# Kernel tuning notes

Hardware: AMD Instinct MI355X
Metric: run time of the kernel (lower is better)

## Reference

```python
import jax, jax.numpy as jnp
import numpy as np

H = 16            # num_heads
WIN = 512         # window_size
G = 64            # num_global_tokens
MAXPOS = 8192


def setup_inputs() -> dict:
    key = jax.random.key(0)
    ks = jax.random.split(key, 9)
    B, S, D = 4, 4096, 1024
    s = 1.0 / np.sqrt(D)
    return {
        "x": jax.random.normal(ks[0], (B, S, D), jnp.float32),
        "pos_emb": jax.random.normal(ks[1], (MAXPOS, D), jnp.float32) * 0.02,
        "global_memory": jax.random.normal(ks[2], (1, G, D), jnp.float32),
        "conv_w": jax.random.normal(ks[3], (D, D, 4), jnp.float32) * s,   # (out_ch, in_ch, k)
        "conv_b": jax.random.normal(ks[4], (D,), jnp.float32) * 0.01,
        "gate_w": jax.random.normal(ks[5], (2 * D, D), jnp.float32) * s,  # (in, out)
        "gate_b": jnp.zeros((D,), jnp.float32),
        "out_w": jax.random.normal(ks[6], (D, D), jnp.float32) * s,
        "out_b": jnp.zeros((D,), jnp.float32),
    }


def reference(x, pos_emb, global_memory, conv_w, conv_b, gate_w, gate_b, out_w, out_b):
    B, S, D = x.shape
    hd = D // H
    scale = 1.0 / np.sqrt(hd)

    # positional encoding (seq <= max_position)
    x = x + pos_emb[:S][None]

    # ---- sliding window attention (non-overlapping windows, q=k=v=x) ----
    pad = (-S) % WIN
    xp = jnp.pad(x, ((0, 0), (0, pad), (0, 0))) if pad else x
    nW = xp.shape[1] // WIN
    w = xp.reshape(B, nW, WIN, H, hd)                                  # [B,nW,W,H,hd]
    attn = jnp.einsum('bnqhd,bnkhd->bnhqk', w, w) * scale
    attn = jax.nn.softmax(attn, axis=-1)
    local = jnp.einsum('bnhqk,bnkhd->bnqhd', attn, w)
    local = local.reshape(B, nW * WIN, D)[:, :S]                       # [B,S,D]

    # ---- compressed global attention ----
    comp = jax.lax.conv_general_dilated(
        x.transpose(0, 2, 1), conv_w, window_strides=(4,), padding='VALID',
        dimension_numbers=('NCH', 'OIH', 'NCH')) + conv_b[None, :, None]
    comp = comp.transpose(0, 2, 1)[:, :G]                              # [B,G,D]
    gt = jnp.concatenate([comp, jnp.broadcast_to(global_memory, (B, G, D))], axis=1)
    gt = gt.reshape(B, 2 * G, H, hd)                                   # [B,2G,H,hd]
    xm = x.reshape(B, S, H, hd)
    ga = jax.nn.softmax(jnp.einsum('bshd,bghd->bhsg', xm, gt) * scale, axis=-1)
    glob = jnp.einsum('bhsg,bghd->bshd', ga, gt).reshape(B, S, D)      # [B,S,D]

    # ---- gated mix + output projection (dropout disabled / eval) ----
    mix = jax.nn.sigmoid(jnp.concatenate([local, glob], axis=-1) @ gate_w + gate_b)
    out = mix * local + (1.0 - mix) * glob
    return out @ out_w + out_b
```

## Files before the change

### kernel.cpp

```cpp
#include <hip/hip_runtime.h>
#include <math.h>

#define B 4
#define S 4096
#define D 1024
#define H 16
#define HD 64
#define WIN 512
#define NW 8
#define G 64
#define G2 128
#define SCALE 0.125f

typedef __attribute__((ext_vector_type(8))) short bf16x8;
typedef __attribute__((ext_vector_type(4))) float f32x4;

__device__ inline unsigned short f2bf(float f) {
    unsigned u = __builtin_bit_cast(unsigned, f);
    return (unsigned short)((u + 0x7FFFu + ((u >> 16) & 1u)) >> 16);
}

__device__ inline float bf2f(unsigned short u) {
    return __builtin_bit_cast(float, (unsigned)u << 16);
}

__device__ inline unsigned long long pack4bf(float a, float b, float c, float d) {
    return (unsigned long long)f2bf(a) | ((unsigned long long)f2bf(b) << 16) |
           ((unsigned long long)f2bf(c) << 32) | ((unsigned long long)f2bf(d) << 48);
}

__device__ inline void gload16(const void* g, void* l) {
    __builtin_amdgcn_global_load_lds(
        (const __attribute__((address_space(1))) unsigned*)g,
        (__attribute__((address_space(3))) unsigned*)l, 16, 0, 0);
}

#define LDS_FENCE() asm volatile("" ::: "memory")

__global__ void k_posadd(const float* __restrict__ x, const float* __restrict__ pos,
                         float* __restrict__ xe) {
    int i = blockIdx.x * blockDim.x + threadIdx.x;
    float4 xv = ((const float4*)x)[i];
    int e = i & (S * D / 4 - 1);
    float4 pv = ((const float4*)pos)[e];
    xv.x += pv.x; xv.y += pv.y; xv.z += pv.z; xv.w += pv.w;
    ((float4*)xe)[i] = xv;
}

template <int KD>
__global__ void k_wtrans(const float* __restrict__ w, unsigned short* __restrict__ wT) {
    __shared__ float tile[32][33];
    int k0 = blockIdx.x * 32, n0 = blockIdx.y * 32;
    int tx = threadIdx.x & 31, ty = threadIdx.x >> 5;
#pragma unroll
    for (int i = 0; i < 4; ++i)
        tile[ty + 8 * i][tx] = w[(size_t)(k0 + ty + 8 * i) * 1024 + n0 + tx];
    __syncthreads();
#pragma unroll
    for (int i = 0; i < 4; ++i)
        wT[(size_t)(n0 + ty + 8 * i) * KD + k0 + tx] = f2bf(tile[tx][ty + 8 * i]);
}

__launch_bounds__(256)
__global__ void k_winattn(const float* __restrict__ xe, unsigned short* __restrict__ local_bf) {
    int blk = blockIdx.x;
    int qt = blk & 3, h = (blk >> 2) & 15, wi = (blk >> 6) & 7, b = blk >> 9;

    __shared__ __align__(16) unsigned char lds[66048];
    unsigned char* Qs = lds;
    unsigned char* Kb = lds + 16384;
    unsigned char* Vb = lds + 32768;
    unsigned char* Pb = lds + 49152;
    float* corr = (float*)(lds + 65536);

    const int t = threadIdx.x;
    const int wv = t >> 6, l = t & 63;
    const int g = l >> 4, c = l & 15;

    const float* wbase = xe + ((size_t)b * S + (size_t)wi * WIN) * D + h * HD;

#pragma unroll
    for (int p = 0; p < 8; ++p) {
        int i = t + 256 * p;
        int q = i >> 4, c4 = i & 15;
        float4 v = *(const float4*)(wbase + (size_t)(qt * 128 + q) * D + c4 * 4);
        *(unsigned long long*)(Qs + q * 128 + ((c4 * 8) ^ ((q & 7) << 4))) =
            pack4bf(v.x * SCALE, v.y * SCALE, v.z * SCALE, v.w * SCALE);
    }

    auto stage_kv = [&](int kt, int bb) {
        unsigned char* kb = Kb + bb * 8192;
        unsigned char* vb = Vb + bb * 8192;
#pragma unroll
        for (int p = 0; p < 4; ++p) {
            int i = t + 256 * p;
            int key = i >> 4, c4 = i & 15;
            float4 v = *(const float4*)(wbase + (size_t)(kt * 64 + key) * D + c4 * 4);
            *(unsigned long long*)(kb + key * 128 + ((c4 * 8) ^ ((key & 7) << 4))) =
                pack4bf(v.x, v.y, v.z, v.w);
            int swz = (c4 & 7) << 4;
            int d0 = c4 * 4;
            *(unsigned short*)(vb + (d0 + 0) * 128 + ((key * 2) ^ swz)) = f2bf(v.x);
            *(unsigned short*)(vb + (d0 + 1) * 128 + ((key * 2) ^ swz)) = f2bf(v.y);
            *(unsigned short*)(vb + (d0 + 2) * 128 + ((key * 2) ^ swz)) = f2bf(v.z);
            *(unsigned short*)(vb + (d0 + 3) * 128 + ((key * 2) ^ swz)) = f2bf(v.w);
        }
    };

    stage_kv(0, 0);
    __syncthreads();

    bf16x8 QB[2][2];
#pragma unroll
    for (int ni = 0; ni < 2; ++ni)
#pragma unroll
        for (int ds = 0; ds < 2; ++ds) {
            int q = wv * 32 + ni * 16 + c;
            QB[ni][ds] = *(const bf16x8*)(Qs + q * 128 + ((ds * 64 + g * 16) ^ ((q & 7) << 4)));
        }

    float m_run[2] = {-1e30f, -1e30f};
    float l_run[2] = {0.f, 0.f};
    f32x4 acc[2][4] = {};
    unsigned char* Pw = Pb + wv * 4096;
    float* corw = corr + wv * 32;

    for (int kt = 0; kt < 8; ++kt) {
        int bb = kt & 1;
        if (kt < 7) stage_kv(kt + 1, bb ^ 1);

        unsigned char* kb = Kb + bb * 8192;
        unsigned char* vb = Vb + bb * 8192;
        bf16x8 KA[4][2];
#pragma unroll
        for (int mi = 0; mi < 4; ++mi)
#pragma unroll
            for (int ds = 0; ds < 2; ++ds) {
                int key = mi * 16 + c;
                KA[mi][ds] = *(const bf16x8*)(kb + key * 128 + ((ds * 64 + g * 16) ^ ((key & 7) << 4)));
            }
        f32x4 sc[4][2] = {};
#pragma unroll
        for (int mi = 0; mi < 4; ++mi)
#pragma unroll
            for (int ni = 0; ni < 2; ++ni) {
                sc[mi][ni] = __builtin_amdgcn_mfma_f32_16x16x32_bf16(KA[mi][0], QB[ni][0], sc[mi][ni], 0, 0, 0);
                sc[mi][ni] = __builtin_amdgcn_mfma_f32_16x16x32_bf16(KA[mi][1], QB[ni][1], sc[mi][ni], 0, 0, 0);
            }
#pragma unroll
        for (int ni = 0; ni < 2; ++ni) {
            float mt = sc[0][ni][0];
#pragma unroll
            for (int mi = 0; mi < 4; ++mi)
#pragma unroll
                for (int r = 0; r < 4; ++r) mt = fmaxf(mt, sc[mi][ni][r]);
            mt = fmaxf(mt, __shfl_xor(mt, 16));
            mt = fmaxf(mt, __shfl_xor(mt, 32));
            float mnew = fmaxf(m_run[ni], mt);
            float co = __expf(m_run[ni] - mnew);
            m_run[ni] = mnew;
            float ps = 0.f;
            int q = ni * 16 + c;
#pragma unroll
            for (int mi = 0; mi < 4; ++mi) {
                float p0 = __expf(sc[mi][ni][0] - mnew);
                float p1 = __expf(sc[mi][ni][1] - mnew);
                float p2 = __expf(sc[mi][ni][2] - mnew);
                float p3 = __expf(sc[mi][ni][3] - mnew);
                ps += (p0 + p1) + (p2 + p3);
                *(unsigned long long*)(Pw + q * 128 + ((2 * (mi * 16 + g * 4)) ^ ((q & 7) << 4))) =
                    pack4bf(p0, p1, p2, p3);
            }
            ps += __shfl_xor(ps, 16);
            ps += __shfl_xor(ps, 32);
            l_run[ni] = l_run[ni] * co + ps;
            if (g == 0) corw[q] = co;
        }
        LDS_FENCE();
#pragma unroll
        for (int mf = 0; mf < 2; ++mf) {
            float cr0 = corw[mf * 16 + g * 4 + 0];
            float cr1 = corw[mf * 16 + g * 4 + 1];
            float cr2 = corw[mf * 16 + g * 4 + 2];
            float cr3 = corw[mf * 16 + g * 4 + 3];
#pragma unroll
            for (int nf = 0; nf < 4; ++nf) {
                acc[mf][nf][0] *= cr0; acc[mf][nf][1] *= cr1;
                acc[mf][nf][2] *= cr2; acc[mf][nf][3] *= cr3;
            }
        }
        bf16x8 PA[2][2], VBf[4][2];
#pragma unroll
        for (int mf = 0; mf < 2; ++mf)
#pragma unroll
            for (int ks = 0; ks < 2; ++ks) {
                int q = mf * 16 + c;
                PA[mf][ks] = *(const bf16x8*)(Pw + q * 128 + ((ks * 64 + g * 16) ^ ((q & 7) << 4)));
            }
#pragma unroll
        for (int nf = 0; nf < 4; ++nf)
#pragma unroll
            for (int ks = 0; ks < 2; ++ks) {
                int d = nf * 16 + c;
                VBf[nf][ks] = *(const bf16x8*)(vb + d * 128 + ((ks * 64 + g * 16) ^ (((d >> 2) & 7) << 4)));
            }
#pragma unroll
        for (int mf = 0; mf < 2; ++mf)
#pragma unroll
            for (int nf = 0; nf < 4; ++nf) {
                acc[mf][nf] = __builtin_amdgcn_mfma_f32_16x16x32_bf16(PA[mf][0], VBf[nf][0], acc[mf][nf], 0, 0, 0);
                acc[mf][nf] = __builtin_amdgcn_mfma_f32_16x16x32_bf16(PA[mf][1], VBf[nf][1], acc[mf][nf], 0, 0, 0);
            }
        __syncthreads();
    }

    if (g == 0) { corw[c] = 1.f / l_run[0]; corw[16 + c] = 1.f / l_run[1]; }
    LDS_FENCE();
#pragma unroll
    for (int mf = 0; mf < 2; ++mf) {
        float iv[4];
#pragma unroll
        for (int r = 0; r < 4; ++r) iv[r] = corw[mf * 16 + g * 4 + r];
#pragma unroll
        for (int r = 0; r < 4; ++r) {
            size_t row = (size_t)b * S + (size_t)wi * WIN + qt * 128 + wv * 32 + mf * 16 + g * 4 + r;
#pragma unroll
            for (int nf = 0; nf < 4; ++nf) {
                int col = h * HD + nf * 16 + c;
                local_bf[row * D + col] = f2bf(acc[mf][nf][r] * iv[r]);
            }
        }
    }
}

__launch_bounds__(256)
__global__ void k_conv_part(const float* __restrict__ xe, const float* __restrict__ convw,
                            float* __restrict__ part) {
    int bid = blockIdx.x;
    int nt = bid & 15, mt = (bid >> 4) & 3, kc = bid >> 6;
    __shared__ float As[32][68];
    __shared__ float Bs[32][68];
    int t = threadIdx.x, tx = t & 15, ty = t >> 4;
    float acc[4][4] = {};
    for (int k0 = 0; k0 < 1024; k0 += 32) {
#pragma unroll
        for (int p = 0; p < 2; ++p) {
            int fidx = t + 256 * p;
            int am = fidx >> 3, ak4 = fidx & 7;
            int bg = mt * 64 + am, b = bg >> 6, g = bg & 63;
            float4 v = *(const float4*)(xe + ((size_t)b * S + 4 * g + kc) * D + k0 + ak4 * 4);
            As[ak4*4+0][am] = v.x; As[ak4*4+1][am] = v.y;
            As[ak4*4+2][am] = v.z; As[ak4*4+3][am] = v.w;
        }
#pragma unroll
        for (int p = 0; p < 8; ++p) {
            int bk = t & 31, bn = (t >> 5) + 8 * p;
            Bs[bk][bn] = convw[(size_t)(nt * 64 + bn) * 4096 + (size_t)(k0 + bk) * 4 + kc];
        }
        __syncthreads();
#pragma unroll
        for (int kk = 0; kk < 32; ++kk) {
            float a[4], bb[4];
            *(float4*)a  = *(const float4*)(&As[kk][ty * 4]);
            *(float4*)bb = *(const float4*)(&Bs[kk][tx * 4]);
#pragma unroll
            for (int i = 0; i < 4; ++i)
#pragma unroll
                for (int j = 0; j < 4; ++j)
                    acc[i][j] = fmaf(a[i], bb[j], acc[i][j]);
        }
        __syncthreads();
    }
#pragma unroll
    for (int i = 0; i < 4; ++i) {
        size_t off = ((size_t)kc * 256 + mt * 64 + ty * 4 + i) * 1024 + nt * 64 + tx * 4;
        *(float4*)(part + off) = make_float4(acc[i][0], acc[i][1], acc[i][2], acc[i][3]);
    }
}

__global__ void k_gt(const float* __restrict__ part, const float* __restrict__ convb,
                     const float* __restrict__ gmem, float* __restrict__ gt) {
    int f = blockIdx.x * blockDim.x + threadIdx.x;
    int n4  = f & 255;
    int tok = (f >> 8) & 127;
    int b   = f >> 15;
    float4 v;
    if (tok < 64) {
        v = ((const float4*)convb)[n4];
#pragma unroll
        for (int kc = 0; kc < 4; ++kc) {
            float4 p = ((const float4*)part)[((size_t)kc * 256 + b * 64 + tok) * 256 + n4];
            v.x += p.x; v.y += p.y; v.z += p.z; v.w += p.w;
        }
    } else {
        v = ((const float4*)gmem)[(size_t)(tok - 64) * 256 + n4];
    }
    ((float4*)gt)[f] = v;
}

__launch_bounds__(256)
__global__ void k_globattn(const float* __restrict__ xe, const float* __restrict__ gt,
                           unsigned short* __restrict__ glob_bf) {
    int blk = blockIdx.x;
    int qt = blk & 31, h = (blk >> 5) & 15, b = blk >> 9;

    __shared__ __align__(16) unsigned char lds[66048];
    unsigned char* Qs = lds;
    unsigned char* Kb = lds + 16384;
    unsigned char* Vb = lds + 32768;
    unsigned char* Pb = lds + 49152;
    float* corr = (float*)(lds + 65536);

    const int t = threadIdx.x;
    const int wv = t >> 6, l = t & 63;
    const int g = l >> 4, c = l & 15;

    const float* qbase  = xe + ((size_t)b * S + (size_t)qt * 128) * D + h * HD;
    const float* kvbase = gt + (size_t)b * G2 * D + h * HD;

#pragma unroll
    for (int p = 0; p < 8; ++p) {
        int i = t + 256 * p;
        int q = i >> 4, c4 = i & 15;
        float4 v = *(const float4*)(qbase + (size_t)q * D + c4 * 4);
        *(unsigned long long*)(Qs + q * 128 + ((c4 * 8) ^ ((q & 7) << 4))) =
            pack4bf(v.x * SCALE, v.y * SCALE, v.z * SCALE, v.w * SCALE);
    }

    auto stage_kv = [&](int kt, int bb) {
        unsigned char* kb = Kb + bb * 8192;
        unsigned char* vb = Vb + bb * 8192;
#pragma unroll
        for (int p = 0; p < 4; ++p) {
            int i = t + 256 * p;
            int key = i >> 4, c4 = i & 15;
            float4 v = *(const float4*)(kvbase + (size_t)(kt * 64 + key) * D + c4 * 4);
            *(unsigned long long*)(kb + key * 128 + ((c4 * 8) ^ ((key & 7) << 4))) =
                pack4bf(v.x, v.y, v.z, v.w);
            int swz = (c4 & 7) << 4;
            int d0 = c4 * 4;
            *(unsigned short*)(vb + (d0 + 0) * 128 + ((key * 2) ^ swz)) = f2bf(v.x);
            *(unsigned short*)(vb + (d0 + 1) * 128 + ((key * 2) ^ swz)) = f2bf(v.y);
            *(unsigned short*)(vb + (d0 + 2) * 128 + ((key * 2) ^ swz)) = f2bf(v.z);
            *(unsigned short*)(vb + (d0 + 3) * 128 + ((key * 2) ^ swz)) = f2bf(v.w);
        }
    };

    stage_kv(0, 0);
    __syncthreads();

    bf16x8 QB[2][2];
#pragma unroll
    for (int ni = 0; ni < 2; ++ni)
#pragma unroll
        for (int ds = 0; ds < 2; ++ds) {
            int q = wv * 32 + ni * 16 + c;
            QB[ni][ds] = *(const bf16x8*)(Qs + q * 128 + ((ds * 64 + g * 16) ^ ((q & 7) << 4)));
        }

    float m_run[2] = {-1e30f, -1e30f};
    float l_run[2] = {0.f, 0.f};
    f32x4 acc[2][4] = {};
    unsigned char* Pw = Pb + wv * 4096;
    float* corw = corr + wv * 32;

    for (int kt = 0; kt < 2; ++kt) {
        int bb = kt & 1;
        if (kt < 1) stage_kv(kt + 1, bb ^ 1);

        unsigned char* kb = Kb + bb * 8192;
        unsigned char* vb = Vb + bb * 8192;
        bf16x8 KA[4][2];
#pragma unroll
        for (int mi = 0; mi < 4; ++mi)
#pragma unroll
            for (int ds = 0; ds < 2; ++ds) {
                int key = mi * 16 + c;
                KA[mi][ds] = *(const bf16x8*)(kb + key * 128 + ((ds * 64 + g * 16) ^ ((key & 7) << 4)));
            }
        f32x4 sc[4][2] = {};
#pragma unroll
        for (int mi = 0; mi < 4; ++mi)
#pragma unroll
            for (int ni = 0; ni < 2; ++ni) {
                sc[mi][ni] = __builtin_amdgcn_mfma_f32_16x16x32_bf16(KA[mi][0], QB[ni][0], sc[mi][ni], 0, 0, 0);
                sc[mi][ni] = __builtin_amdgcn_mfma_f32_16x16x32_bf16(KA[mi][1], QB[ni][1], sc[mi][ni], 0, 0, 0);
            }
#pragma unroll
        for (int ni = 0; ni < 2; ++ni) {
            float mt = sc[0][ni][0];
#pragma unroll
            for (int mi = 0; mi < 4; ++mi)
#pragma unroll
                for (int r = 0; r < 4; ++r) mt = fmaxf(mt, sc[mi][ni][r]);
            mt = fmaxf(mt, __shfl_xor(mt, 16));
            mt = fmaxf(mt, __shfl_xor(mt, 32));
            float mnew = fmaxf(m_run[ni], mt);
            float co = __expf(m_run[ni] - mnew);
            m_run[ni] = mnew;
            float ps = 0.f;
            int q = ni * 16 + c;
#pragma unroll
            for (int mi = 0; mi < 4; ++mi) {
                float p0 = __expf(sc[mi][ni][0] - mnew);
                float p1 = __expf(sc[mi][ni][1] - mnew);
                float p2 = __expf(sc[mi][ni][2] - mnew);
                float p3 = __expf(sc[mi][ni][3] - mnew);
                ps += (p0 + p1) + (p2 + p3);
                *(unsigned long long*)(Pw + q * 128 + ((2 * (mi * 16 + g * 4)) ^ ((q & 7) << 4))) =
                    pack4bf(p0, p1, p2, p3);
            }
            ps += __shfl_xor(ps, 16);
            ps += __shfl_xor(ps, 32);
            l_run[ni] = l_run[ni] * co + ps;
            if (g == 0) corw[q] = co;
        }
        LDS_FENCE();
#pragma unroll
        for (int mf = 0; mf < 2; ++mf) {
            float cr0 = corw[mf * 16 + g * 4 + 0];
            float cr1 = corw[mf * 16 + g * 4 + 1];
            float cr2 = corw[mf * 16 + g * 4 + 2];
            float cr3 = corw[mf * 16 + g * 4 + 3];
#pragma unroll
            for (int nf = 0; nf < 4; ++nf) {
                acc[mf][nf][0] *= cr0; acc[mf][nf][1] *= cr1;
                acc[mf][nf][2] *= cr2; acc[mf][nf][3] *= cr3;
            }
        }
        bf16x8 PA[2][2], VBf[4][2];
#pragma unroll
        for (int mf = 0; mf < 2; ++mf)
#pragma unroll
            for (int ks = 0; ks < 2; ++ks) {
                int q = mf * 16 + c;
                PA[mf][ks] = *(const bf16x8*)(Pw + q * 128 + ((ks * 64 + g * 16) ^ ((q & 7) << 4)));
            }
#pragma unroll
        for (int nf = 0; nf < 4; ++nf)
#pragma unroll
            for (int ks = 0; ks < 2; ++ks) {
                int d = nf * 16 + c;
                VBf[nf][ks] = *(const bf16x8*)(vb + d * 128 + ((ks * 64 + g * 16) ^ (((d >> 2) & 7) << 4)));
            }
#pragma unroll
        for (int mf = 0; mf < 2; ++mf)
#pragma unroll
            for (int nf = 0; nf < 4; ++nf) {
                acc[mf][nf] = __builtin_amdgcn_mfma_f32_16x16x32_bf16(PA[mf][0], VBf[nf][0], acc[mf][nf], 0, 0, 0);
                acc[mf][nf] = __builtin_amdgcn_mfma_f32_16x16x32_bf16(PA[mf][1], VBf[nf][1], acc[mf][nf], 0, 0, 0);
            }
        __syncthreads();
    }

    if (g == 0) { corw[c] = 1.f / l_run[0]; corw[16 + c] = 1.f / l_run[1]; }
    LDS_FENCE();
#pragma unroll
    for (int mf = 0; mf < 2; ++mf) {
        float iv[4];
#pragma unroll
        for (int r = 0; r < 4; ++r) iv[r] = corw[mf * 16 + g * 4 + r];
#pragma unroll
        for (int r = 0; r < 4; ++r) {
            size_t row = (size_t)b * S + (size_t)qt * 128 + wv * 32 + mf * 16 + g * 4 + r;
#pragma unroll
            for (int nf = 0; nf < 4; ++nf) {
                int col = h * HD + nf * 16 + c;
                glob_bf[row * D + col] = f2bf(acc[mf][nf][r] * iv[r]);
            }
        }
    }
}

template <int MODE>
__launch_bounds__(256)
__global__ void k_mgemm(const unsigned short* __restrict__ A0,
                        const unsigned short* __restrict__ A1,
                        const unsigned short* __restrict__ BT,
                        const float* __restrict__ bias,
                        void* __restrict__ Cout) {
    constexpr int K = (MODE == 0) ? 2048 : 1024;
    __shared__ __align__(16) unsigned short As[128 * 32];
    __shared__ __align__(16) unsigned short Bs[128 * 32];
    const int t = threadIdx.x;
    const int wv = t >> 6, ln = t & 63;
    const int lrow = ln & 15, lk = ln >> 4;
    const int wr = wv >> 1, wc = wv & 1;

    int lin = blockIdx.x;
    int swz = (lin & 7) * 128 + (lin >> 3);
    const int bn = (swz & 7) * 128;
    const int bm = (swz >> 3) * 128;

    const int arow = ln >> 2;
    const int acol8 = (ln & 3) * 8;

    f32x4 acc[4][4] = {};

    for (int k0 = 0; k0 < K; k0 += 32) {
        const unsigned short* Ab;
        int kloc;
        if constexpr (MODE == 0) { Ab = (k0 < 1024) ? A0 : A1; kloc = k0 & 1023; }
        else                     { Ab = A0; kloc = k0; }
        gload16(Ab + (size_t)(bm + wv * 32 + arow) * 1024 + kloc + acol8,
                As + wv * 32 * 32);
        gload16(Ab + (size_t)(bm + wv * 32 + 16 + arow) * 1024 + kloc + acol8,
                As + wv * 32 * 32 + 16 * 32);
        gload16(BT + (size_t)(bn + wv * 32 + arow) * K + k0 + acol8,
                Bs + wv * 32 * 32);
        gload16(BT + (size_t)(bn + wv * 32 + 16 + arow) * K + k0 + acol8,
                Bs + wv * 32 * 32 + 16 * 32);
        __syncthreads();
        bf16x8 af[4], bfr[4];
#pragma unroll
        for (int m = 0; m < 4; ++m)
            af[m] = *(const bf16x8*)(As + (wr * 64 + m * 16 + lrow) * 32 + lk * 8);
#pragma unroll
        for (int n = 0; n < 4; ++n)
            bfr[n] = *(const bf16x8*)(Bs + (wc * 64 + n * 16 + lrow) * 32 + lk * 8);
#pragma unroll
        for (int m = 0; m < 4; ++m)
#pragma unroll
            for (int n = 0; n < 4; ++n)
                acc[m][n] = __builtin_amdgcn_mfma_f32_16x16x32_bf16(af[m], bfr[n], acc[m][n], 0, 0, 0);
        __syncthreads();
    }

#pragma unroll
    for (int m = 0; m < 4; ++m) {
#pragma unroll
        for (int n = 0; n < 4; ++n) {
            int col = bn + wc * 64 + n * 16 + lrow;
            float bv = bias[col];
#pragma unroll
            for (int r = 0; r < 4; ++r) {
                int row = bm + wr * 64 + m * 16 + lk * 4 + r;
                size_t off = (size_t)row * 1024 + col;
                float v = acc[m][n][r] + bv;
                if constexpr (MODE == 0) {
                    float mixv = 1.f / (1.f + __expf(-v));
                    float o = mixv * bf2f(A0[off]) + (1.f - mixv) * bf2f(A1[off]);
                    ((unsigned short*)Cout)[off] = f2bf(o);
                } else {
                    ((float*)Cout)[off] = v;
                }
            }
        }
    }
}

extern "C" void kernel_launch(void* const* d_in, const int* in_sizes, int n_in,
                              void* d_out, int out_size, void* d_ws, size_t ws_size,
                              hipStream_t stream) {
    (void)in_sizes; (void)n_in; (void)out_size; (void)ws_size;
    const float* x     = (const float*)d_in[0];
    const float* pos   = (const float*)d_in[1];
    const float* gmem  = (const float*)d_in[2];
    const float* convw = (const float*)d_in[3];
    const float* convb = (const float*)d_in[4];
    const float* gatew = (const float*)d_in[5];
    const float* gateb = (const float*)d_in[6];
    const float* outw  = (const float*)d_in[7];
    const float* outb  = (const float*)d_in[8];

    float* ws = (float*)d_ws;
    float* xe    = ws;
    float* hole  = xe + 16777216;
    float* gt    = hole + 16777216;
    float* part  = gt + 524288;
    unsigned short* local_bf = (unsigned short*)(part + 1048576);
    unsigned short* glob_bf  = local_bf + 16777216;
    unsigned short* wTg      = glob_bf + 16777216;
    unsigned short* wTo      = wTg + 2097152;
    unsigned short* mixed_bf = (unsigned short*)xe;

    k_posadd  <<<16384, 256, 0, stream>>>(x, pos, xe);
    k_wtrans<2048><<<dim3(64, 32), 256, 0, stream>>>(gatew, wTg);
    k_wtrans<1024><<<dim3(32, 32), 256, 0, stream>>>(outw, wTo);
    k_winattn <<<B * NW * H * 4, 256, 0, stream>>>(xe, local_bf);
    k_conv_part<<<256, 256, 0, stream>>>(xe, convw, part);
    k_gt      <<<512, 256, 0, stream>>>(part, convb, gmem, gt);
    k_globattn<<<B * H * (S / 128), 256, 0, stream>>>(xe, gt, glob_bf);
    k_mgemm<0><<<1024, 256, 0, stream>>>(local_bf, glob_bf, wTg, gateb, mixed_bf);
    k_mgemm<1><<<1024, 256, 0, stream>>>(mixed_bf, nullptr, wTo, outb, d_out);
}
```

Baseline: 515.3 us.

## Fuse positional add into consumers, remap winattn blocks per XCD, widen GEMM K-tile

```diff
diff --git a/kernel.cpp b/kernel.cpp
--- a/kernel.cpp
+++ b/kernel.cpp
@@ -37,16 +37,6 @@
 
 #define LDS_FENCE() asm volatile("" ::: "memory")
 
-__global__ void k_posadd(const float* __restrict__ x, const float* __restrict__ pos,
-                         float* __restrict__ xe) {
-    int i = blockIdx.x * blockDim.x + threadIdx.x;
-    float4 xv = ((const float4*)x)[i];
-    int e = i & (S * D / 4 - 1);
-    float4 pv = ((const float4*)pos)[e];
-    xv.x += pv.x; xv.y += pv.y; xv.z += pv.z; xv.w += pv.w;
-    ((float4*)xe)[i] = xv;
-}
-
 template <int KD>
 __global__ void k_wtrans(const float* __restrict__ w, unsigned short* __restrict__ wT) {
     __shared__ float tile[32][33];
@@ -62,9 +52,14 @@
 }
 
 __launch_bounds__(256)
-__global__ void k_winattn(const float* __restrict__ xe, unsigned short* __restrict__ local_bf) {
+__global__ void k_winattn(const float* __restrict__ x, const float* __restrict__ pos,
+                          unsigned short* __restrict__ local_bf) {
     int blk = blockIdx.x;
-    int qt = blk & 3, h = (blk >> 2) & 15, wi = (blk >> 6) & 7, b = blk >> 9;
+    int xcd = blk & 7, rest = blk >> 3;
+    int g2 = xcd * 4 + (rest >> 6);
+    int inner = rest & 63;
+    int qt = inner & 3, h = inner >> 2;
+    int wi = g2 & 7, b = g2 >> 3;
 
     __shared__ __align__(16) unsigned char lds[66048];
     unsigned char* Qs = lds;
@@ -77,13 +72,17 @@
     const int wv = t >> 6, l = t & 63;
     const int g = l >> 4, c = l & 15;
 
-    const float* wbase = xe + ((size_t)b * S + (size_t)wi * WIN) * D + h * HD;
+    const float* xb = x + ((size_t)b * S + (size_t)wi * WIN) * D + h * HD;
+    const float* pb = pos + (size_t)wi * WIN * D + h * HD;
 
 #pragma unroll
     for (int p = 0; p < 8; ++p) {
         int i = t + 256 * p;
         int q = i >> 4, c4 = i & 15;
-        float4 v = *(const float4*)(wbase + (size_t)(qt * 128 + q) * D + c4 * 4);
+        size_t off = (size_t)(qt * 128 + q) * D + c4 * 4;
+        float4 v = *(const float4*)(xb + off);
+        float4 pv = *(const float4*)(pb + off);
+        v.x += pv.x; v.y += pv.y; v.z += pv.z; v.w += pv.w;
         *(unsigned long long*)(Qs + q * 128 + ((c4 * 8) ^ ((q & 7) << 4))) =
             pack4bf(v.x * SCALE, v.y * SCALE, v.z * SCALE, v.w * SCALE);
     }
@@ -95,7 +94,10 @@
         for (int p = 0; p < 4; ++p) {
             int i = t + 256 * p;
             int key = i >> 4, c4 = i & 15;
-            float4 v = *(const float4*)(wbase + (size_t)(kt * 64 + key) * D + c4 * 4);
+            size_t off = (size_t)(kt * 64 + key) * D + c4 * 4;
+            float4 v = *(const float4*)(xb + off);
+            float4 pv = *(const float4*)(pb + off);
+            v.x += pv.x; v.y += pv.y; v.z += pv.z; v.w += pv.w;
             *(unsigned long long*)(kb + key * 128 + ((c4 * 8) ^ ((key & 7) << 4))) =
                 pack4bf(v.x, v.y, v.z, v.w);
             int swz = (c4 & 7) << 4;
@@ -234,8 +236,8 @@
 }
 
 __launch_bounds__(256)
-__global__ void k_conv_part(const float* __restrict__ xe, const float* __restrict__ convw,
-                            float* __restrict__ part) {
+__global__ void k_conv_part(const float* __restrict__ x, const float* __restrict__ pos,
+                            const float* __restrict__ convw, float* __restrict__ part) {
     int bid = blockIdx.x;
     int nt = bid & 15, mt = (bid >> 4) & 3, kc = bid >> 6;
     __shared__ float As[32][68];
@@ -248,7 +250,9 @@
             int fidx = t + 256 * p;
             int am = fidx >> 3, ak4 = fidx & 7;
             int bg = mt * 64 + am, b = bg >> 6, g = bg & 63;
-            float4 v = *(const float4*)(xe + ((size_t)b * S + 4 * g + kc) * D + k0 + ak4 * 4);
+            float4 v = *(const float4*)(x + ((size_t)b * S + 4 * g + kc) * D + k0 + ak4 * 4);
+            float4 pv = *(const float4*)(pos + (size_t)(4 * g + kc) * D + k0 + ak4 * 4);
+            v.x += pv.x; v.y += pv.y; v.z += pv.z; v.w += pv.w;
             As[ak4*4+0][am] = v.x; As[ak4*4+1][am] = v.y;
             As[ak4*4+2][am] = v.z; As[ak4*4+3][am] = v.w;
         }
@@ -299,8 +303,8 @@
 }
 
 __launch_bounds__(256)
-__global__ void k_globattn(const float* __restrict__ xe, const float* __restrict__ gt,
-                           unsigned short* __restrict__ glob_bf) {
+__global__ void k_globattn(const float* __restrict__ x, const float* __restrict__ pos,
+                           const float* __restrict__ gt, unsigned short* __restrict__ glob_bf) {
     int blk = blockIdx.x;
     int qt = blk & 31, h = (blk >> 5) & 15, b = blk >> 9;
 
@@ -315,14 +319,18 @@
     const int wv = t >> 6, l = t & 63;
     const int g = l >> 4, c = l & 15;
 
-    const float* qbase  = xe + ((size_t)b * S + (size_t)qt * 128) * D + h * HD;
+    const float* qbx = x + ((size_t)b * S + (size_t)qt * 128) * D + h * HD;
+    const float* qbp = pos + (size_t)qt * 128 * D + h * HD;
     const float* kvbase = gt + (size_t)b * G2 * D + h * HD;
 
 #pragma unroll
     for (int p = 0; p < 8; ++p) {
         int i = t + 256 * p;
         int q = i >> 4, c4 = i & 15;
-        float4 v = *(const float4*)(qbase + (size_t)q * D + c4 * 4);
+        size_t off = (size_t)q * D + c4 * 4;
+        float4 v = *(const float4*)(qbx + off);
+        float4 pv = *(const float4*)(qbp + off);
+        v.x += pv.x; v.y += pv.y; v.z += pv.z; v.w += pv.w;
         *(unsigned long long*)(Qs + q * 128 + ((c4 * 8) ^ ((q & 7) << 4))) =
             pack4bf(v.x * SCALE, v.y * SCALE, v.z * SCALE, v.w * SCALE);
     }
@@ -480,8 +488,8 @@
                         const float* __restrict__ bias,
                         void* __restrict__ Cout) {
     constexpr int K = (MODE == 0) ? 2048 : 1024;
-    __shared__ __align__(16) unsigned short As[128 * 32];
-    __shared__ __align__(16) unsigned short Bs[128 * 32];
+    __shared__ __align__(16) unsigned short As[128 * 64];
+    __shared__ __align__(16) unsigned short Bs[128 * 64];
     const int t = threadIdx.x;
     const int wv = t >> 6, ln = t & 63;
     const int lrow = ln & 15, lk = ln >> 4;
@@ -492,37 +500,47 @@
     const int bn = (swz & 7) * 128;
     const int bm = (swz >> 3) * 128;
 
-    const int arow = ln >> 2;
-    const int acol8 = (ln & 3) * 8;
+    const int srow = ln >> 3;
+    const int schunk = ((ln & 7) ^ (ln >> 3)) * 8;
 
     f32x4 acc[4][4] = {};
 
-    for (int k0 = 0; k0 < K; k0 += 32) {
+    for (int k0 = 0; k0 < K; k0 += 64) {
         const unsigned short* Ab;
         int kloc;
         if constexpr (MODE == 0) { Ab = (k0 < 1024) ? A0 : A1; kloc = k0 & 1023; }
         else                     { Ab = A0; kloc = k0; }
-        gload16(Ab + (size_t)(bm + wv * 32 + arow) * 1024 + kloc + acol8,
-                As + wv * 32 * 32);
-        gload16(Ab + (size_t)(bm + wv * 32 + 16 + arow) * 1024 + kloc + acol8,
-                As + wv * 32 * 32 + 16 * 32);
-        gload16(BT + (size_t)(bn + wv * 32 + arow) * K + k0 + acol8,
-                Bs + wv * 32 * 32);
-        gload16(BT + (size_t)(bn + wv * 32 + 16 + arow) * K + k0 + acol8,
-                Bs + wv * 32 * 32 + 16 * 32);
+#pragma unroll
+        for (int j = 0; j < 4; ++j) {
+            int r0 = wv * 32 + j * 8;
+            gload16(Ab + (size_t)(bm + r0 + srow) * 1024 + kloc + schunk, As + r0 * 64);
+            gload16(BT + (size_t)(bn + r0 + srow) * K + k0 + schunk,      Bs + r0 * 64);
+        }
         __syncthreads();
-        bf16x8 af[4], bfr[4];
+        bf16x8 af[4][2], bfr[4][2];
+#pragma unroll
+        for (int m = 0; m < 4; ++m) {
+            int row = wr * 64 + m * 16 + lrow;
+#pragma unroll
+            for (int ks = 0; ks < 2; ++ks)
+                af[m][ks] = *(const bf16x8*)((const unsigned char*)As + row * 128 +
+                                ((ks * 64 + lk * 16) ^ ((row & 7) << 4)));
+        }
+#pragma unroll
+        for (int n = 0; n < 4; ++n) {
+            int row = wc * 64 + n * 16 + lrow;
+#pragma unroll
+            for (int ks = 0; ks < 2; ++ks)
+                bfr[n][ks] = *(const bf16x8*)((const unsigned char*)Bs + row * 128 +
+                                ((ks * 64 + lk * 16) ^ ((row & 7) << 4)));
+        }
 #pragma unroll
         for (int m = 0; m < 4; ++m)
-            af[m] = *(const bf16x8*)(As + (wr * 64 + m * 16 + lrow) * 32 + lk * 8);
-#pragma unroll
-        for (int n = 0; n < 4; ++n)
-            bfr[n] = *(const bf16x8*)(Bs + (wc * 64 + n * 16 + lrow) * 32 + lk * 8);
-#pragma unroll
-        for (int m = 0; m < 4; ++m)
-#pragma unroll
-            for (int n = 0; n < 4; ++n)
-                acc[m][n] = __builtin_amdgcn_mfma_f32_16x16x32_bf16(af[m], bfr[n], acc[m][n], 0, 0, 0);
+#pragma unroll
+            for (int n = 0; n < 4; ++n) {
+                acc[m][n] = __builtin_amdgcn_mfma_f32_16x16x32_bf16(af[m][0], bfr[n][0], acc[m][n], 0, 0, 0);
+                acc[m][n] = __builtin_amdgcn_mfma_f32_16x16x32_bf16(af[m][1], bfr[n][1], acc[m][n], 0, 0, 0);
+            }
         __syncthreads();
     }
 
@@ -564,23 +582,20 @@
     const float* outb  = (const float*)d_in[8];
 
     float* ws = (float*)d_ws;
-    float* xe    = ws;
-    float* hole  = xe + 16777216;
-    float* gt    = hole + 16777216;
-    float* part  = gt + 524288;
+    float* gt   = ws;
+    float* part = gt + 524288;
     unsigned short* local_bf = (unsigned short*)(part + 1048576);
     unsigned short* glob_bf  = local_bf + 16777216;
-    unsigned short* wTg      = glob_bf + 16777216;
+    unsigned short* mixed_bf = glob_bf + 16777216;
+    unsigned short* wTg      = mixed_bf + 16777216;
     unsigned short* wTo      = wTg + 2097152;
-    unsigned short* mixed_bf = (unsigned short*)xe;
-
-    k_posadd  <<<16384, 256, 0, stream>>>(x, pos, xe);
+
     k_wtrans<2048><<<dim3(64, 32), 256, 0, stream>>>(gatew, wTg);
     k_wtrans<1024><<<dim3(32, 32), 256, 0, stream>>>(outw, wTo);
-    k_winattn <<<B * NW * H * 4, 256, 0, stream>>>(xe, local_bf);
-    k_conv_part<<<256, 256, 0, stream>>>(xe, convw, part);
+    k_winattn <<<B * NW * H * 4, 256, 0, stream>>>(x, pos, local_bf);
+    k_conv_part<<<256, 256, 0, stream>>>(x, pos, convw, part);
     k_gt      <<<512, 256, 0, stream>>>(part, convb, gmem, gt);
-    k_globattn<<<B * H * (S / 128), 256, 0, stream>>>(xe, gt, glob_bf);
+    k_globattn<<<B * H * (S / 128), 256, 0, stream>>>(x, pos, gt, glob_bf);
     k_mgemm<0><<<1024, 256, 0, stream>>>(local_bf, glob_bf, wTg, gateb, mixed_bf);
     k_mgemm<1><<<1024, 256, 0, stream>>>(mixed_bf, nullptr, wTo, outb, d_out);
 }
```

Result: faster. 504.7 us (-2.1%).
